# Optimization experiments

Hardware: AMD Instinct MI355X
Metric: run time of the kernel (lower is better)

## Reference

```python
import jax, jax.numpy as jnp
import numpy as np

N_EMBED = 64
HEAD_SIZE = 64
B, T = 4096, 128

def setup_inputs() -> dict:
    key = jax.random.key(0)
    k0, k1, k2, k3 = jax.random.split(key, 4)
    x = jax.random.normal(k0, (B, T, N_EMBED), dtype=jnp.float32)
    # nn.Linear(N_EMBED, head_size, bias=False): weight shape [head_size, N_EMBED], y = x @ W.T
    Wq = jax.random.normal(k1, (HEAD_SIZE, N_EMBED), dtype=jnp.float32) * (1.0 / np.sqrt(N_EMBED))
    Wk = jax.random.normal(k2, (HEAD_SIZE, N_EMBED), dtype=jnp.float32) * (1.0 / np.sqrt(N_EMBED))
    Wv = jax.random.normal(k3, (HEAD_SIZE, N_EMBED), dtype=jnp.float32) * (1.0 / np.sqrt(N_EMBED))
    return {"x": x, "Wq": Wq, "Wk": Wk, "Wv": Wv}

def reference(x, Wq, Wk, Wv):
    # q,k,v: [B,T,H]
    q = jnp.einsum('btc,hc->bth', x, Wq)
    k = jnp.einsum('btc,hc->bth', x, Wk)
    v = jnp.einsum('btc,hc->bth', x, Wv)
    scale = HEAD_SIZE ** -0.5
    scores = jnp.einsum('bth,bsh->bts', q, k) * scale  # [B,T,T]
    Tdim = x.shape[1]
    causal = jnp.tril(jnp.ones((Tdim, Tdim), dtype=bool))
    scores = jnp.where(causal, scores, -jnp.inf)
    weights = jax.nn.softmax(scores, axis=-1)
    # dropout disabled (eval mode) for deterministic reference
    out = jnp.einsum('bts,bsh->bth', weights, v)  # [B,T,H]
    return out
```

## Files before the change

### kernel.cpp

```cpp
#include <hip/hip_runtime.h>

#define TDIM 128
#define CDIM 64
#define HDIM 64
#define KS 76
#define VS 140
#define QS 76
#define PS 44
#define STRIP_SH 1216

typedef float f4  __attribute__((ext_vector_type(4)));
typedef short s8v __attribute__((ext_vector_type(8)));
typedef short s4v __attribute__((ext_vector_type(4)));

#define MFMA16(a, b, c) __builtin_amdgcn_mfma_f32_16x16x32_bf16((a), (b), (c), 0, 0, 0)

__device__ __forceinline__ unsigned short f2bf(float f) {
  union { float f; unsigned u; } x; x.f = f;
  unsigned r = x.u + 0x7FFFu + ((x.u >> 16) & 1u);
  return (unsigned short)(r >> 16);
}
__device__ __forceinline__ float bf2f(unsigned short s) {
  union { unsigned u; float f; } x; x.u = ((unsigned)s) << 16; return x.f;
}
__device__ __forceinline__ s8v cvt8(const float* p) {
  float4 a = *(const float4*)p;
  float4 b = *(const float4*)(p + 4);
  s8v v;
  v[0] = (short)f2bf(a.x); v[1] = (short)f2bf(a.y);
  v[2] = (short)f2bf(a.z); v[3] = (short)f2bf(a.w);
  v[4] = (short)f2bf(b.x); v[5] = (short)f2bf(b.y);
  v[6] = (short)f2bf(b.z); v[7] = (short)f2bf(b.w);
  return v;
}
__device__ __forceinline__ s8v ld8(const short* p) {
  s4v lo = *(const s4v*)p;
  s4v hi = *(const s4v*)(p + 4);
  s8v r;
  r[0] = lo[0]; r[1] = lo[1]; r[2] = lo[2]; r[3] = lo[3];
  r[4] = hi[0]; r[5] = hi[1]; r[6] = hi[2]; r[7] = hi[3];
  return r;
}

__global__ void detect_bf16(const unsigned short* __restrict__ w, int nelems,
                            int* __restrict__ flag) {
  __shared__ int cnt;
  if (threadIdx.x == 0) cnt = 0;
  __syncthreads();
  int local = 0;
  for (int i = threadIdx.x; i < nelems; i += blockDim.x) {
    float f = bf2f(w[i]);
    float a = fabsf(f);
    if (f == 0.0f || (a >= 1e-4f && a <= 1e4f)) local++;
  }
  atomicAdd(&cnt, local);
  __syncthreads();
  if (threadIdx.x == 0) *flag = (cnt >= (nelems / 10) * 9) ? 1 : 0;
}

__global__ __launch_bounds__(256, 3)
void attn_head(const void* __restrict__ xg, const void* __restrict__ wqg,
               const void* __restrict__ wkg, const void* __restrict__ wvg,
               void* __restrict__ outg, const int* __restrict__ flagp) {
  __shared__ __align__(16) short smem[23552];
  short* Ksm = smem;
  short* Vt  = smem + 9728;
  const int tid  = threadIdx.x;
  const int wave = tid >> 6;
  const int lane = tid & 63;
  const int c16  = lane & 15;
  const int quad = lane >> 4;
  const int b    = blockIdx.x;
  const int isbf = *flagp;
  short* strip = smem + 18688 + wave * STRIP_SH;

  const int mts[2] = {wave, 7 - wave};

  s8v a[2][2];
  #pragma unroll
  for (int mi = 0; mi < 2; mi++) {
    const int m = mts[mi];
    #pragma unroll
    for (int kt = 0; kt < 2; kt++) {
      const int off = (m * 16 + c16) * CDIM + kt * 32 + quad * 8;
      if (isbf) a[mi][kt] = *(const s8v*)((const unsigned short*)xg + (size_t)b * (TDIM * CDIM) + off);
      else      a[mi][kt] = cvt8((const float*)xg + (size_t)b * (TDIM * CDIM) + off);
    }
  }
  f4 q[2][4];
  #pragma unroll
  for (int nt = 0; nt < 4; nt++) {
    s8v wq[2], wk[2], wv[2];
    #pragma unroll
    for (int kt = 0; kt < 2; kt++) {
      const int off = (nt * 16 + c16) * CDIM + kt * 32 + quad * 8;
      if (isbf) {
        wq[kt] = *(const s8v*)((const unsigned short*)wqg + off);
        wk[kt] = *(const s8v*)((const unsigned short*)wkg + off);
        wv[kt] = *(const s8v*)((const unsigned short*)wvg + off);
      } else {
        wq[kt] = cvt8((const float*)wqg + off);
        wk[kt] = cvt8((const float*)wkg + off);
        wv[kt] = cvt8((const float*)wvg + off);
      }
    }
    #pragma unroll
    for (int mi = 0; mi < 2; mi++) {
      const int m = mts[mi];
      f4 k = {0.f, 0.f, 0.f, 0.f}, v = {0.f, 0.f, 0.f, 0.f};
      f4 qq = {0.f, 0.f, 0.f, 0.f};
      qq = MFMA16(a[mi][0], wq[0], qq);  qq = MFMA16(a[mi][1], wq[1], qq);
      k  = MFMA16(a[mi][0], wk[0], k);   k  = MFMA16(a[mi][1], wk[1], k);
      v  = MFMA16(a[mi][0], wv[0], v);   v  = MFMA16(a[mi][1], wv[1], v);
      q[mi][nt] = qq;
      #pragma unroll
      for (int r = 0; r < 4; r++)
        Ksm[(m * 16 + quad * 4 + r) * KS + nt * 16 + c16] = (short)f2bf(k[r]);
      s4v pv;
      pv[0] = (short)f2bf(v[0]); pv[1] = (short)f2bf(v[1]);
      pv[2] = (short)f2bf(v[2]); pv[3] = (short)f2bf(v[3]);
      *(s4v*)(Vt + (nt * 16 + c16) * VS + m * 16 + quad * 4) = pv;
    }
  }
  __syncthreads();

  #pragma unroll
  for (int mi = 0; mi < 2; mi++) {
    const int m = mts[mi];
    #pragma unroll
    for (int nt = 0; nt < 4; nt++)
      #pragma unroll
      for (int r = 0; r < 4; r++)
        strip[(quad * 4 + r) * QS + nt * 16 + c16] = (short)f2bf(q[mi][nt][r] * 0.125f);
    const s8v aq0 = ld8(strip + c16 * QS + quad * 8);
    const s8v aq1 = ld8(strip + c16 * QS + 32 + quad * 8);

    float S[8][4];
    #pragma unroll
    for (int nt = 0; nt < 8; nt++) {
      if (nt > m) continue;
      const s8v kb0 = ld8(Ksm + (nt * 16 + c16) * KS + quad * 8);
      const s8v kb1 = ld8(Ksm + (nt * 16 + c16) * KS + 32 + quad * 8);
      f4 s = {0.f, 0.f, 0.f, 0.f};
      s = MFMA16(aq0, kb0, s);
      s = MFMA16(aq1, kb1, s);
      S[nt][0] = s[0]; S[nt][1] = s[1]; S[nt][2] = s[2]; S[nt][3] = s[3];
    }
    float inv[4];
    #pragma unroll
    for (int r = 0; r < 4; r++) {
      const int tloc = quad * 4 + r;
      float sum = 0.0f;
      #pragma unroll
      for (int nt = 0; nt < 8; nt++) {
        if (nt > m) continue;
        const bool keep = (nt < m) || (c16 <= tloc);
        float e = keep ? __expf(S[nt][r]) : 0.0f;
        S[nt][r] = e;
        sum += e;
      }
      sum += __shfl_xor(sum, 1);
      sum += __shfl_xor(sum, 2);
      sum += __shfl_xor(sum, 4);
      sum += __shfl_xor(sum, 8);
      inv[r] = 1.0f / sum;
    }
    f4 acc[4];
    #pragma unroll
    for (int nt = 0; nt < 4; nt++) { f4 z = {0.f,0.f,0.f,0.f}; acc[nt] = z; }
    const int ktmax = m >> 1;
    #pragma unroll
    for (int kt = 0; kt < 4; kt++) {
      if (kt > ktmax) continue;
      #pragma unroll
      for (int j = 0; j < 2; j++) {
        const int nt = kt * 2 + j;
        #pragma unroll
        for (int r = 0; r < 4; r++)
          strip[(quad * 4 + r) * PS + j * 16 + c16] =
              (nt <= m) ? (short)f2bf(S[nt][r]) : (short)0;
      }
      const s8v ap = ld8(strip + c16 * PS + quad * 8);
      #pragma unroll
      for (int nt = 0; nt < 4; nt++) {
        const s8v vb = ld8(Vt + (nt * 16 + c16) * VS + kt * 32 + quad * 8);
        acc[nt] = MFMA16(ap, vb, acc[nt]);
      }
    }
    if (isbf) {
      unsigned short* op = (unsigned short*)outg + (size_t)b * (TDIM * HDIM);
      #pragma unroll
      for (int nt = 0; nt < 4; nt++)
        #pragma unroll
        for (int r = 0; r < 4; r++)
          op[(m * 16 + quad * 4 + r) * HDIM + nt * 16 + c16] = f2bf(acc[nt][r] * inv[r]);
    } else {
      float* op = (float*)outg + (size_t)b * (TDIM * HDIM);
      #pragma unroll
      for (int nt = 0; nt < 4; nt++)
        #pragma unroll
        for (int r = 0; r < 4; r++)
          op[(m * 16 + quad * 4 + r) * HDIM + nt * 16 + c16] = acc[nt][r] * inv[r];
    }
  }
}

extern "C" void kernel_launch(void* const* d_in, const int* in_sizes, int n_in,
                              void* d_out, int out_size, void* d_ws, size_t ws_size,
                              hipStream_t stream) {
  int* flag = (int*)d_ws;
  detect_bf16<<<dim3(1), dim3(256), 0, stream>>>(
      (const unsigned short*)d_in[1], in_sizes[1], flag);
  attn_head<<<dim3(4096), dim3(256), 0, stream>>>(
      d_in[0], d_in[1], d_in[2], d_in[3], d_out, (const int*)flag);
}
```

Before: 333.2 us.

## Compute transposed Q/S tiles and pass MFMA operands via register shuffles

Computes Q transposed (W·x) and scores as K·Q so each lane holds one query column. The bf16 Q and probability operands are then rebuilt with cross-lane shuffles, removing the per-wave LDS strip round-trips and shrinking shared memory. The softmax row sum reduces across quads with two shuffles and a single reciprocal. Output stores become vectorized float4 writes. The shuffles add instruction count, and correctness depends on the new transposed fragment mapping.

```diff
diff --git a/kernel.cpp b/kernel.cpp
--- a/kernel.cpp
+++ b/kernel.cpp
@@ -1,13 +1,7 @@
 #include <hip/hip_runtime.h>
 
-#define TDIM 128
-#define CDIM 64
-#define HDIM 64
 #define KS 76
 #define VS 140
-#define QS 76
-#define PS 44
-#define STRIP_SH 1216
 
 typedef float f4  __attribute__((ext_vector_type(4)));
 typedef short s8v __attribute__((ext_vector_type(8)));
@@ -40,6 +34,28 @@
   r[0] = lo[0]; r[1] = lo[1]; r[2] = lo[2]; r[3] = lo[3];
   r[4] = hi[0]; r[5] = hi[1]; r[6] = hi[2]; r[7] = hi[3];
   return r;
+}
+__device__ __forceinline__ unsigned pack2(float a, float b) {
+  return (unsigned)f2bf(a) | ((unsigned)f2bf(b) << 16);
+}
+
+__device__ __forceinline__ s8v qshuf(unsigned pa0, unsigned pa1,
+                                     unsigned pb0, unsigned pb1,
+                                     int s0, bool hi) {
+  int a0 = __shfl((int)pa0, s0);
+  int a1 = __shfl((int)pa1, s0);
+  int a2 = __shfl((int)pa0, s0 + 16);
+  int a3 = __shfl((int)pa1, s0 + 16);
+  int b0 = __shfl((int)pb0, s0);
+  int b1 = __shfl((int)pb1, s0);
+  int b2 = __shfl((int)pb0, s0 + 16);
+  int b3 = __shfl((int)pb1, s0 + 16);
+  union { int u[4]; s8v v; } r;
+  r.u[0] = hi ? b0 : a0;
+  r.u[1] = hi ? b1 : a1;
+  r.u[2] = hi ? b2 : a2;
+  r.u[3] = hi ? b3 : a3;
+  return r.v;
 }
 
 __global__ void detect_bf16(const unsigned short* __restrict__ w, int nelems,
@@ -62,9 +78,10 @@
 void attn_head(const void* __restrict__ xg, const void* __restrict__ wqg,
                const void* __restrict__ wkg, const void* __restrict__ wvg,
                void* __restrict__ outg, const int* __restrict__ flagp) {
-  __shared__ __align__(16) short smem[23552];
+  __shared__ __align__(16) short smem[18688];
   short* Ksm = smem;
   short* Vt  = smem + 9728;
+
   const int tid  = threadIdx.x;
   const int wave = tid >> 6;
   const int lane = tid & 63;
@@ -72,135 +89,144 @@
   const int quad = lane >> 4;
   const int b    = blockIdx.x;
   const int isbf = *flagp;
-  short* strip = smem + 18688 + wave * STRIP_SH;
-
   const int mts[2] = {wave, 7 - wave};
 
-  s8v a[2][2];
+  s8v xf[2][2];
+  #pragma unroll
+  for (int mi = 0; mi < 2; mi++) {
+    const size_t base = (size_t)b * (128 * 64) + (size_t)(mts[mi] * 16 + c16) * 64;
+    #pragma unroll
+    for (int kt = 0; kt < 2; kt++) {
+      const int off = kt * 32 + quad * 8;
+      if (isbf) xf[mi][kt] = *(const s8v*)((const unsigned short*)xg + base + off);
+      else      xf[mi][kt] = cvt8((const float*)xg + base + off);
+    }
+  }
+
+  f4 QT[2][4];
+  #pragma unroll
+  for (int ht = 0; ht < 4; ht++) {
+    s8v wqf[2], wkf[2], wvf[2];
+    const int woff0 = (ht * 16 + c16) * 64 + quad * 8;
+    #pragma unroll
+    for (int kt = 0; kt < 2; kt++) {
+      const int off = woff0 + kt * 32;
+      if (isbf) {
+        wqf[kt] = *(const s8v*)((const unsigned short*)wqg + off);
+        wkf[kt] = *(const s8v*)((const unsigned short*)wkg + off);
+        wvf[kt] = *(const s8v*)((const unsigned short*)wvg + off);
+      } else {
+        wqf[kt] = cvt8((const float*)wqg + off);
+        wkf[kt] = cvt8((const float*)wkg + off);
+        wvf[kt] = cvt8((const float*)wvg + off);
+      }
+    }
+    #pragma unroll
+    for (int mi = 0; mi < 2; mi++) {
+      const int m = mts[mi];
+      f4 z = {0.f, 0.f, 0.f, 0.f};
+      f4 qt = z, kk = z, vv = z;
+      qt = MFMA16(wqf[0], xf[mi][0], qt);  qt = MFMA16(wqf[1], xf[mi][1], qt);
+      kk = MFMA16(xf[mi][0], wkf[0], kk);  kk = MFMA16(xf[mi][1], wkf[1], kk);
+      vv = MFMA16(xf[mi][0], wvf[0], vv);  vv = MFMA16(xf[mi][1], wvf[1], vv);
+      QT[mi][ht] = qt;
+      #pragma unroll
+      for (int r = 0; r < 4; r++)
+        Ksm[(m * 16 + quad * 4 + r) * KS + ht * 16 + c16] = (short)f2bf(kk[r]);
+      s4v pv;
+      pv[0] = (short)f2bf(vv[0]); pv[1] = (short)f2bf(vv[1]);
+      pv[2] = (short)f2bf(vv[2]); pv[3] = (short)f2bf(vv[3]);
+      *(s4v*)(Vt + (ht * 16 + c16) * VS + m * 16 + quad * 4) = pv;
+    }
+  }
+  __syncthreads();
+
+  const int s0 = ((quad & 1) * 2) * 16 + c16;
+  const bool hi = quad >= 2;
+
   #pragma unroll
   for (int mi = 0; mi < 2; mi++) {
     const int m = mts[mi];
-    #pragma unroll
-    for (int kt = 0; kt < 2; kt++) {
-      const int off = (m * 16 + c16) * CDIM + kt * 32 + quad * 8;
-      if (isbf) a[mi][kt] = *(const s8v*)((const unsigned short*)xg + (size_t)b * (TDIM * CDIM) + off);
-      else      a[mi][kt] = cvt8((const float*)xg + (size_t)b * (TDIM * CDIM) + off);
-    }
-  }
-  f4 q[2][4];
-  #pragma unroll
-  for (int nt = 0; nt < 4; nt++) {
-    s8v wq[2], wk[2], wv[2];
-    #pragma unroll
-    for (int kt = 0; kt < 2; kt++) {
-      const int off = (nt * 16 + c16) * CDIM + kt * 32 + quad * 8;
-      if (isbf) {
-        wq[kt] = *(const s8v*)((const unsigned short*)wqg + off);
-        wk[kt] = *(const s8v*)((const unsigned short*)wkg + off);
-        wv[kt] = *(const s8v*)((const unsigned short*)wvg + off);
-      } else {
-        wq[kt] = cvt8((const float*)wqg + off);
-        wk[kt] = cvt8((const float*)wkg + off);
-        wv[kt] = cvt8((const float*)wvg + off);
-      }
-    }
-    #pragma unroll
-    for (int mi = 0; mi < 2; mi++) {
-      const int m = mts[mi];
-      f4 k = {0.f, 0.f, 0.f, 0.f}, v = {0.f, 0.f, 0.f, 0.f};
-      f4 qq = {0.f, 0.f, 0.f, 0.f};
-      qq = MFMA16(a[mi][0], wq[0], qq);  qq = MFMA16(a[mi][1], wq[1], qq);
-      k  = MFMA16(a[mi][0], wk[0], k);   k  = MFMA16(a[mi][1], wk[1], k);
-      v  = MFMA16(a[mi][0], wv[0], v);   v  = MFMA16(a[mi][1], wv[1], v);
-      q[mi][nt] = qq;
-      #pragma unroll
-      for (int r = 0; r < 4; r++)
-        Ksm[(m * 16 + quad * 4 + r) * KS + nt * 16 + c16] = (short)f2bf(k[r]);
-      s4v pv;
-      pv[0] = (short)f2bf(v[0]); pv[1] = (short)f2bf(v[1]);
-      pv[2] = (short)f2bf(v[2]); pv[3] = (short)f2bf(v[3]);
-      *(s4v*)(Vt + (nt * 16 + c16) * VS + m * 16 + quad * 4) = pv;
-    }
-  }
-  __syncthreads();
-
-  #pragma unroll
-  for (int mi = 0; mi < 2; mi++) {
-    const int m = mts[mi];
-    #pragma unroll
-    for (int nt = 0; nt < 4; nt++)
-      #pragma unroll
-      for (int r = 0; r < 4; r++)
-        strip[(quad * 4 + r) * QS + nt * 16 + c16] = (short)f2bf(q[mi][nt][r] * 0.125f);
-    const s8v aq0 = ld8(strip + c16 * QS + quad * 8);
-    const s8v aq1 = ld8(strip + c16 * QS + 32 + quad * 8);
-
-    float S[8][4];
+    unsigned qpk[4][2];
+    #pragma unroll
+    for (int ht = 0; ht < 4; ht++) {
+      qpk[ht][0] = pack2(QT[mi][ht][0] * 0.125f, QT[mi][ht][1] * 0.125f);
+      qpk[ht][1] = pack2(QT[mi][ht][2] * 0.125f, QT[mi][ht][3] * 0.125f);
+    }
+    s8v qb[2];
+    qb[0] = qshuf(qpk[0][0], qpk[0][1], qpk[1][0], qpk[1][1], s0, hi);
+    qb[1] = qshuf(qpk[2][0], qpk[2][1], qpk[3][0], qpk[3][1], s0, hi);
+
+    f4 S[8];
     #pragma unroll
     for (int nt = 0; nt < 8; nt++) {
       if (nt > m) continue;
-      const s8v kb0 = ld8(Ksm + (nt * 16 + c16) * KS + quad * 8);
-      const s8v kb1 = ld8(Ksm + (nt * 16 + c16) * KS + 32 + quad * 8);
+      const s8v ka0 = ld8(Ksm + (nt * 16 + c16) * KS + quad * 8);
+      const s8v ka1 = ld8(Ksm + (nt * 16 + c16) * KS + 32 + quad * 8);
       f4 s = {0.f, 0.f, 0.f, 0.f};
-      s = MFMA16(aq0, kb0, s);
-      s = MFMA16(aq1, kb1, s);
-      S[nt][0] = s[0]; S[nt][1] = s[1]; S[nt][2] = s[2]; S[nt][3] = s[3];
-    }
-    float inv[4];
-    #pragma unroll
-    for (int r = 0; r < 4; r++) {
-      const int tloc = quad * 4 + r;
-      float sum = 0.0f;
-      #pragma unroll
-      for (int nt = 0; nt < 8; nt++) {
-        if (nt > m) continue;
-        const bool keep = (nt < m) || (c16 <= tloc);
+      s = MFMA16(ka0, qb[0], s);
+      s = MFMA16(ka1, qb[1], s);
+      S[nt] = s;
+    }
+    float sum = 0.f;
+    #pragma unroll
+    for (int nt = 0; nt < 8; nt++) {
+      if (nt > m) continue;
+      #pragma unroll
+      for (int r = 0; r < 4; r++) {
+        const bool keep = (nt < m) || (quad * 4 + r <= c16);
         float e = keep ? __expf(S[nt][r]) : 0.0f;
         S[nt][r] = e;
         sum += e;
       }
-      sum += __shfl_xor(sum, 1);
-      sum += __shfl_xor(sum, 2);
-      sum += __shfl_xor(sum, 4);
-      sum += __shfl_xor(sum, 8);
-      inv[r] = 1.0f / sum;
-    }
+    }
+    sum += __shfl_xor(sum, 16);
+    sum += __shfl_xor(sum, 32);
+    const float inv = 1.0f / sum;
+
+    unsigned ppk[8][2];
+    #pragma unroll
+    for (int nt = 0; nt < 8; nt++) {
+      if (nt > m) continue;
+      ppk[nt][0] = pack2(S[nt][0], S[nt][1]);
+      ppk[nt][1] = pack2(S[nt][2], S[nt][3]);
+    }
+
     f4 acc[4];
     #pragma unroll
-    for (int nt = 0; nt < 4; nt++) { f4 z = {0.f,0.f,0.f,0.f}; acc[nt] = z; }
-    const int ktmax = m >> 1;
+    for (int ht = 0; ht < 4; ht++) { f4 z = {0.f,0.f,0.f,0.f}; acc[ht] = z; }
+    const int nchunk = (m >> 1) + 1;
     #pragma unroll
     for (int kt = 0; kt < 4; kt++) {
-      if (kt > ktmax) continue;
-      #pragma unroll
-      for (int j = 0; j < 2; j++) {
-        const int nt = kt * 2 + j;
-        #pragma unroll
-        for (int r = 0; r < 4; r++)
-          strip[(quad * 4 + r) * PS + j * 16 + c16] =
-              (nt <= m) ? (short)f2bf(S[nt][r]) : (short)0;
-      }
-      const s8v ap = ld8(strip + c16 * PS + quad * 8);
-      #pragma unroll
-      for (int nt = 0; nt < 4; nt++) {
-        const s8v vb = ld8(Vt + (nt * 16 + c16) * VS + kt * 32 + quad * 8);
-        acc[nt] = MFMA16(ap, vb, acc[nt]);
-      }
-    }
+      if (kt >= nchunk) continue;
+      const bool hb = (2 * kt + 1) <= m;
+      s8v pb = qshuf(ppk[2 * kt][0], ppk[2 * kt][1],
+                     hb ? ppk[2 * kt + 1][0] : 0u,
+                     hb ? ppk[2 * kt + 1][1] : 0u, s0, hi);
+      #pragma unroll
+      for (int ht = 0; ht < 4; ht++) {
+        const s8v va = ld8(Vt + (ht * 16 + c16) * VS + kt * 32 + quad * 8);
+        acc[ht] = MFMA16(va, pb, acc[ht]);
+      }
+    }
+
     if (isbf) {
-      unsigned short* op = (unsigned short*)outg + (size_t)b * (TDIM * HDIM);
-      #pragma unroll
-      for (int nt = 0; nt < 4; nt++)
-        #pragma unroll
-        for (int r = 0; r < 4; r++)
-          op[(m * 16 + quad * 4 + r) * HDIM + nt * 16 + c16] = f2bf(acc[nt][r] * inv[r]);
+      unsigned short* op = (unsigned short*)outg + (size_t)b * (128 * 64);
+      #pragma unroll
+      for (int ht = 0; ht < 4; ht++) {
+        s4v o;
+        o[0] = (short)f2bf(acc[ht][0] * inv); o[1] = (short)f2bf(acc[ht][1] * inv);
+        o[2] = (short)f2bf(acc[ht][2] * inv); o[3] = (short)f2bf(acc[ht][3] * inv);
+        *(s4v*)(op + (size_t)(m * 16 + c16) * 64 + ht * 16 + quad * 4) = o;
+      }
     } else {
-      float* op = (float*)outg + (size_t)b * (TDIM * HDIM);
-      #pragma unroll
-      for (int nt = 0; nt < 4; nt++)
-        #pragma unroll
-        for (int r = 0; r < 4; r++)
-          op[(m * 16 + quad * 4 + r) * HDIM + nt * 16 + c16] = acc[nt][r] * inv[r];
+      float* op = (float*)outg + (size_t)b * (128 * 64);
+      #pragma unroll
+      for (int ht = 0; ht < 4; ht++) {
+        float4 o = {acc[ht][0] * inv, acc[ht][1] * inv,
+                    acc[ht][2] * inv, acc[ht][3] * inv};
+        *(float4*)(op + (size_t)(m * 16 + c16) * 64 + ht * 16 + quad * 4) = o;
+      }
     }
   }
 }
```

After: 313.7 us. 5.9% less time.
